# Kernel tuning notes

Hardware: AMD Instinct MI355X
Metric: run time of the kernel (lower is better)

The kernel has to match this reference:

```python
import jax, jax.numpy as jnp
import numpy as np

DIM = 1024
HEADS = 16
DIM_HEAD = 64
INNER = HEADS * DIM_HEAD  # 1024
FF_INNER = 4 * DIM        # 4096
EPS = 1e-5


def _ln(t, gamma):
    mu = jnp.mean(t, axis=-1, keepdims=True)
    var = jnp.var(t, axis=-1, keepdims=True)
    return (t - mu) * jax.lax.rsqrt(var + EPS) * gamma


def setup_inputs() -> dict:
    key = jax.random.key(0)
    ks = jax.random.split(key, 8)
    B, N = 4, 1024
    s = 0.02
    return {
        "x": jax.random.normal(ks[0], (B, N, DIM), dtype=jnp.float32),
        "y": jax.random.normal(ks[1], (B, N, DIM), dtype=jnp.float32),
        "g1": jnp.ones((DIM,), dtype=jnp.float32),
        "g2": jnp.ones((DIM,), dtype=jnp.float32),
        "g_out": jnp.ones((DIM,), dtype=jnp.float32),
        "Wq": jax.random.normal(ks[2], (DIM, INNER), dtype=jnp.float32) * s,
        "Wkv": jax.random.normal(ks[3], (DIM, 2 * DIM_HEAD), dtype=jnp.float32) * s,
        "Wo": jax.random.normal(ks[4], (INNER, DIM), dtype=jnp.float32) * s,
        "Wff1": jax.random.normal(ks[5], (DIM, 2 * FF_INNER), dtype=jnp.float32) * s,
        "Wff2": jax.random.normal(ks[6], (FF_INNER, DIM), dtype=jnp.float32) * s,
    }


def reference(x, y, g1, g2, g_out, Wq, Wkv, Wo, Wff1, Wff2):
    B, N, _ = x.shape
    scale = DIM_HEAD ** -0.5
    xn = _ln(x, g1)
    yn = _ln(y, g2)  # note: torch code rebinds y = norm2(y); residual & FF use normed y
    # multi-query attention: per-head queries, single shared k/v head
    q = (xn @ Wq).reshape(B, N, HEADS, DIM_HEAD).transpose(0, 2, 1, 3) * scale  # b h n d
    kv = yn @ Wkv  # b j (2d)
    k, v = kv[..., :DIM_HEAD], kv[..., DIM_HEAD:]
    sim = jnp.einsum('bhid,bjd->bhij', q, k)
    attn = jax.nn.softmax(sim, axis=-1)  # torch code subtracts amax then softmax; identical math
    out = jnp.einsum('bhij,bjd->bhid', attn, v)
    out = out.transpose(0, 2, 1, 3).reshape(B, N, INNER)
    out = out @ Wo
    out = _ln(out + yn, g_out)
    # SwiGLU FFN on normed y: first half is value, second half is gate
    h = yn @ Wff1
    val, gate = h[..., :FF_INNER], h[..., FF_INNER:]
    ff = (jax.nn.silu(gate) * val) @ Wff2
    return out + ff
```

## Files before the change

### kernel.cpp

```cpp
#include <hip/hip_runtime.h>
#include <hip/hip_bf16.h>


typedef __attribute__((ext_vector_type(8))) short bf16x8;
typedef __attribute__((ext_vector_type(4))) short s16x4;
typedef __attribute__((ext_vector_type(4))) float f32x4;

__device__ __forceinline__ short f2b(float f) {
  union { float f; unsigned u; } v; v.f = f;
  unsigned r = (v.u + 0x7fffu + ((v.u >> 16) & 1u)) >> 16;
  return (short)r;
}

__device__ __forceinline__ void gload16(const short* g, short* l) {
  __builtin_amdgcn_global_load_lds(
      (const __attribute__((address_space(1))) void*)g,
      (__attribute__((address_space(3))) void*)l, 16, 0, 0);
}

__global__ __launch_bounds__(256) void cvtT_kernel(const float* __restrict__ in,
                                                   short* __restrict__ out,
                                                   int K, int N) {
  __shared__ float tile[32][33];
  int n0 = blockIdx.x * 32, k0 = blockIdx.y * 32;
  int tx = threadIdx.x & 7, ty = threadIdx.x >> 3;
  float4 v = *(const float4*)&in[(size_t)(k0 + ty) * N + n0 + tx * 4];
  tile[ty][tx * 4 + 0] = v.x;
  tile[ty][tx * 4 + 1] = v.y;
  tile[ty][tx * 4 + 2] = v.z;
  tile[ty][tx * 4 + 3] = v.w;
  __syncthreads();
  s16x4 o = { f2b(tile[tx * 4 + 0][ty]), f2b(tile[tx * 4 + 1][ty]),
              f2b(tile[tx * 4 + 2][ty]), f2b(tile[tx * 4 + 3][ty]) };
  *(s16x4*)&out[(size_t)(n0 + ty) * K + k0 + tx * 4] = o;
}

__global__ __launch_bounds__(256) void ln_kernel(const float* __restrict__ in,
                                                 const float* __restrict__ gamma,
                                                 short* __restrict__ out16,
                                                 float* __restrict__ out32) {
  int row = blockIdx.x;
  int t = threadIdx.x;
  float4 v = ((const float4*)(in + (size_t)row * 1024))[t];
  float s  = v.x + v.y + v.z + v.w;
  float sq = v.x*v.x + v.y*v.y + v.z*v.z + v.w*v.w;
  __shared__ float ssum[256], ssq[256];
  ssum[t] = s; ssq[t] = sq;
  __syncthreads();
  for (int o = 128; o > 0; o >>= 1) {
    if (t < o) { ssum[t] += ssum[t + o]; ssq[t] += ssq[t + o]; }
    __syncthreads();
  }
  float mu  = ssum[0] * (1.0f / 1024.0f);
  float var = ssq[0] * (1.0f / 1024.0f) - mu * mu;
  float rs  = rsqrtf(var + 1e-5f);
  float4 g = ((const float4*)gamma)[t];
  float o0 = (v.x - mu) * rs * g.x;
  float o1 = (v.y - mu) * rs * g.y;
  float o2 = (v.z - mu) * rs * g.z;
  float o3 = (v.w - mu) * rs * g.w;
  if (out16) {
    s16x4 o = { f2b(o0), f2b(o1), f2b(o2), f2b(o3) };
    ((s16x4*)out16)[(size_t)row * 256 + t] = o;
  }
  if (out32) {
    float4 o = { o0, o1, o2, o3 };
    ((float4*)out32)[(size_t)row * 256 + t] = o;
  }
}

template<int EPI, int BM, int BN>
__global__ __launch_bounds__(256, 2) void gemm_ring(
    const short* __restrict__ A, const short* __restrict__ B,
    int M, int N, int Kstride, int Klen,
    short* __restrict__ out16, float* __restrict__ out32,
    const float* __restrict__ res, float scale)
{
  constexpr int DEPTH = 4;
  constexpr int FM = BM / 32;
  constexpr int FN = BN / 32;
  constexpr int AL = BM / 64;
  constexpr int BL = BN / 64;
  __shared__ __align__(16) short As[DEPTH][BM * 32];
  __shared__ __align__(16) short Bs[DEPTH][BN * 32];

  int t = threadIdx.x;
  int lane = t & 63, wave = t >> 6;
  int wm = wave >> 1, wn = wave & 1;
  int lrow = lane & 15, lgrp = lane >> 4;
  int m0 = blockIdx.y * BM, n0 = blockIdx.x * BN;
  int kbase = blockIdx.z * Klen;

  int srow = lane >> 2, scol = (lane & 3) * 8;
  const short* gA = A + (size_t)(m0 + wave * 16 + srow) * Kstride + kbase + scol;
  const short* gB = B + (size_t)(n0 + wave * 16 + srow) * Kstride + kbase + scol;

  auto STAGE = [&](int slot, int kt) {
    int k0 = kt * 32;
#pragma unroll
    for (int i = 0; i < AL; i++)
      gload16(gA + (size_t)(i * 64) * Kstride + k0, &As[slot][(i * 4 + wave) * 512]);
#pragma unroll
    for (int j = 0; j < BL; j++)
      gload16(gB + (size_t)(j * 64) * Kstride + k0, &Bs[slot][(j * 4 + wave) * 512]);
  };

  f32x4 acc[FM][FN];
  const f32x4 zero = { 0.f, 0.f, 0.f, 0.f };
#pragma unroll
  for (int i = 0; i < FM; i++)
#pragma unroll
    for (int j = 0; j < FN; j++) acc[i][j] = zero;

  int nt = Klen / 32;
#pragma unroll
  for (int p = 0; p < DEPTH - 1; p++) STAGE(p, p);

  int slot = 0, stage_slot = DEPTH - 1;
  for (int tI = 0; tI < nt; ++tI) {
    int rem = nt - 1 - tI;
    if constexpr (AL + BL == 4) {
      if (rem >= 2)      asm volatile("s_waitcnt vmcnt(8)" ::: "memory");
      else if (rem == 1) asm volatile("s_waitcnt vmcnt(4)" ::: "memory");
      else               asm volatile("s_waitcnt vmcnt(0)" ::: "memory");
    } else {
      if (rem >= 2)      asm volatile("s_waitcnt vmcnt(6)" ::: "memory");
      else if (rem == 1) asm volatile("s_waitcnt vmcnt(3)" ::: "memory");
      else               asm volatile("s_waitcnt vmcnt(0)" ::: "memory");
    }
    __builtin_amdgcn_s_barrier();
    __builtin_amdgcn_sched_barrier(0);

    if (tI + DEPTH - 1 < nt) STAGE(stage_slot, tI + DEPTH - 1);

    bf16x8 af[FM], bfr[FN];
#pragma unroll
    for (int mf = 0; mf < FM; mf++)
      af[mf] = *(const bf16x8*)&As[slot][(wm * (BM / 2) + mf * 16 + lrow) * 32 + lgrp * 8];
#pragma unroll
    for (int nf = 0; nf < FN; nf++)
      bfr[nf] = *(const bf16x8*)&Bs[slot][(wn * (BN / 2) + nf * 16 + lrow) * 32 + lgrp * 8];

    __builtin_amdgcn_s_setprio(1);
#pragma unroll
    for (int mf = 0; mf < FM; mf++)
#pragma unroll
      for (int nf = 0; nf < FN; nf++)
        acc[mf][nf] = __builtin_amdgcn_mfma_f32_16x16x32_bf16(af[mf], bfr[nf], acc[mf][nf], 0, 0, 0);
    __builtin_amdgcn_s_setprio(0);

    slot = (slot + 1 == DEPTH) ? 0 : slot + 1;
    stage_slot = (stage_slot + 1 == DEPTH) ? 0 : stage_slot + 1;
  }

#pragma unroll
  for (int mf = 0; mf < FM; mf++)
#pragma unroll
    for (int nf = 0; nf < FN; nf++)
#pragma unroll
      for (int r = 0; r < 4; r++) {
        int row = m0 + wm * (BM / 2) + mf * 16 + lgrp * 4 + r;
        int col = n0 + wn * (BN / 2) + nf * 16 + lrow;
        float v = acc[mf][nf][r];
        if (EPI == 0) {
          out16[(size_t)row * N + col] = f2b(v * scale);
        } else if (EPI == 1) {
          out32[(size_t)row * N + col] = v + res[(size_t)row * N + col];
        } else {
          out32[(size_t)blockIdx.z * M * N + (size_t)row * N + col] = v;
        }
      }
}

__global__ __launch_bounds__(256, 2) void gemm_ff1(
    const short* __restrict__ A, const short* __restrict__ B,
    short* __restrict__ out16)
{
  constexpr int K = 1024, NT = 16;
  __shared__ __align__(16) short As[2][128 * 64];
  __shared__ __align__(16) short Bv[2][64 * 64];
  __shared__ __align__(16) short Bg[2][64 * 64];

  int t = threadIdx.x;
  int lane = t & 63, wave = t >> 6;
  int wm = wave >> 1, wn = wave & 1;
  int lrow = lane & 15, lgrp = lane >> 4;
  int m0 = blockIdx.y * 128, n0 = blockIdx.x * 64;

  int r8 = lane >> 3;
  int schunk = ((lane & 7) ^ r8) * 8;
  const short* gA  = A + (size_t)(m0 + wave * 32 + r8) * K + schunk;
  const short* gBv = B + (size_t)(n0 + wave * 16 + r8) * K + schunk;
  const short* gBg = B + (size_t)(4096 + n0 + wave * 16 + r8) * K + schunk;

  auto STAGE = [&](int buf, int kt) {
    int k0 = kt * 64;
    gload16(gA + k0,                   &As[buf][(wave * 32 + 0) * 64]);
    gload16(gA + (size_t)8 * K + k0,   &As[buf][(wave * 32 + 8) * 64]);
    gload16(gA + (size_t)16 * K + k0,  &As[buf][(wave * 32 + 16) * 64]);
    gload16(gA + (size_t)24 * K + k0,  &As[buf][(wave * 32 + 24) * 64]);
    gload16(gBv + k0,                  &Bv[buf][(wave * 16 + 0) * 64]);
    gload16(gBv + (size_t)8 * K + k0,  &Bv[buf][(wave * 16 + 8) * 64]);
    gload16(gBg + k0,                  &Bg[buf][(wave * 16 + 0) * 64]);
    gload16(gBg + (size_t)8 * K + k0,  &Bg[buf][(wave * 16 + 8) * 64]);
  };

  f32x4 acc[4][2], acc2[4][2];
  const f32x4 zero = { 0.f, 0.f, 0.f, 0.f };
#pragma unroll
  for (int i = 0; i < 4; i++) {
    acc[i][0] = zero; acc[i][1] = zero; acc2[i][0] = zero; acc2[i][1] = zero;
  }

  int rc0 = ((lgrp) ^ (lrow & 7)) * 8;
  int rc1 = ((4 | lgrp) ^ (lrow & 7)) * 8;

  STAGE(0, 0);

  for (int tI = 0; tI < NT; ++tI) {
    int cur = tI & 1, nxt = cur ^ 1;

    asm volatile("s_waitcnt vmcnt(0)" ::: "memory");
    __builtin_amdgcn_s_barrier();
    __builtin_amdgcn_sched_barrier(0);

    if (tI + 1 < NT) STAGE(nxt, tI + 1);

    bf16x8 af0[4], af1[4], bvf[2], bgf[2];
#pragma unroll
    for (int mf = 0; mf < 4; mf++)
      af0[mf] = *(const bf16x8*)&As[cur][(wm * 64 + mf * 16 + lrow) * 64 + rc0];
    bvf[0] = *(const bf16x8*)&Bv[cur][(wn * 32 + lrow) * 64 + rc0];
    bvf[1] = *(const bf16x8*)&Bv[cur][(wn * 32 + 16 + lrow) * 64 + rc0];
    __builtin_amdgcn_s_setprio(1);
#pragma unroll
    for (int mf = 0; mf < 4; mf++) {
      acc[mf][0] = __builtin_amdgcn_mfma_f32_16x16x32_bf16(af0[mf], bvf[0], acc[mf][0], 0, 0, 0);
      acc[mf][1] = __builtin_amdgcn_mfma_f32_16x16x32_bf16(af0[mf], bvf[1], acc[mf][1], 0, 0, 0);
    }
#pragma unroll
    for (int mf = 0; mf < 4; mf++)
      af1[mf] = *(const bf16x8*)&As[cur][(wm * 64 + mf * 16 + lrow) * 64 + rc1];
    bvf[0] = *(const bf16x8*)&Bv[cur][(wn * 32 + lrow) * 64 + rc1];
    bvf[1] = *(const bf16x8*)&Bv[cur][(wn * 32 + 16 + lrow) * 64 + rc1];
#pragma unroll
    for (int mf = 0; mf < 4; mf++) {
      acc[mf][0] = __builtin_amdgcn_mfma_f32_16x16x32_bf16(af1[mf], bvf[0], acc[mf][0], 0, 0, 0);
      acc[mf][1] = __builtin_amdgcn_mfma_f32_16x16x32_bf16(af1[mf], bvf[1], acc[mf][1], 0, 0, 0);
    }
    bgf[0] = *(const bf16x8*)&Bg[cur][(wn * 32 + lrow) * 64 + rc0];
    bgf[1] = *(const bf16x8*)&Bg[cur][(wn * 32 + 16 + lrow) * 64 + rc0];
#pragma unroll
    for (int mf = 0; mf < 4; mf++) {
      acc2[mf][0] = __builtin_amdgcn_mfma_f32_16x16x32_bf16(af0[mf], bgf[0], acc2[mf][0], 0, 0, 0);
      acc2[mf][1] = __builtin_amdgcn_mfma_f32_16x16x32_bf16(af0[mf], bgf[1], acc2[mf][1], 0, 0, 0);
    }
    bgf[0] = *(const bf16x8*)&Bg[cur][(wn * 32 + lrow) * 64 + rc1];
    bgf[1] = *(const bf16x8*)&Bg[cur][(wn * 32 + 16 + lrow) * 64 + rc1];
#pragma unroll
    for (int mf = 0; mf < 4; mf++) {
      acc2[mf][0] = __builtin_amdgcn_mfma_f32_16x16x32_bf16(af1[mf], bgf[0], acc2[mf][0], 0, 0, 0);
      acc2[mf][1] = __builtin_amdgcn_mfma_f32_16x16x32_bf16(af1[mf], bgf[1], acc2[mf][1], 0, 0, 0);
    }
    __builtin_amdgcn_s_setprio(0);
  }

#pragma unroll
  for (int mf = 0; mf < 4; mf++)
#pragma unroll
    for (int nf = 0; nf < 2; nf++)
#pragma unroll
      for (int r = 0; r < 4; r++) {
        int row = m0 + wm * 64 + mf * 16 + lgrp * 4 + r;
        int col = n0 + wn * 32 + nf * 16 + lrow;
        float v = acc[mf][nf][r];
        float gate = acc2[mf][nf][r];
        float sig = 1.0f / (1.0f + __expf(-gate));
        out16[(size_t)row * 4096 + col] = f2b(v * gate * sig);
      }
}

__global__ __launch_bounds__(256) void kvred_kernel(const float* __restrict__ p,
                                                    short* __restrict__ out,
                                                    short* __restrict__ vT) {
  int i = blockIdx.x * 256 + threadIdx.x;
  const int S = 4096 * 128 / 4;
  float4 a = ((const float4*)p)[i];
  float4 b = ((const float4*)p)[i + S];
  float4 c = ((const float4*)p)[i + 2 * S];
  float4 d = ((const float4*)p)[i + 3 * S];
  s16x4 o = { f2b(a.x + b.x + c.x + d.x), f2b(a.y + b.y + c.y + d.y),
              f2b(a.z + b.z + c.z + d.z), f2b(a.w + b.w + c.w + d.w) };
  ((s16x4*)out)[i] = o;
  int row = i >> 5, col4 = i & 31;
  if (col4 >= 16) {
    int bb = row >> 10, n = row & 1023;
    int dbase = col4 * 4 - 64;
    short* vt = vT + ((size_t)(bb * 64 + dbase)) * 1024 + n;
    vt[0]        = o[0];
    vt[1024]     = o[1];
    vt[2048]     = o[2];
    vt[3072]     = o[3];
  }
}

__global__ __launch_bounds__(256) void attn_kernel(const short* __restrict__ q,
                                                   const short* __restrict__ kv,
                                                   const short* __restrict__ vT,
                                                   short* __restrict__ ao)
{
  __shared__ __align__(16) short Ks[2][64 * 64];
  __shared__ __align__(16) short Vt[2][64 * 64];
  __shared__ __align__(16) short Ps[4][32 * 64];

  int t = threadIdx.x;
  int lane = t & 63, wave = t >> 6;
  int lrow = lane & 15, lgrp = lane >> 4;
  int qt = blockIdx.x;
  int b = blockIdx.y >> 2, hg = blockIdx.y & 3;
  int h = hg * 4 + wave;

  char* Pb = (char*)Ps + wave * (32 * 64 * 2);

  int r8 = lane >> 3;
  int schunk = ((lane & 7) ^ r8) * 8;
  const short* gK = kv + ((size_t)(b * 1024 + wave * 16 + r8)) * 128 + schunk;
  const short* gV = vT + ((size_t)(b * 64 + wave * 16 + r8)) * 1024 + schunk;

  auto STAGE = [&](int buf, int j0) {
    gload16(gK + (size_t)(j0 + 0) * 128, &Ks[buf][(wave * 16 + 0) * 64]);
    gload16(gK + (size_t)(j0 + 8) * 128, &Ks[buf][(wave * 16 + 8) * 64]);
    gload16(gV + j0,                     &Vt[buf][(wave * 16 + 0) * 64]);
    gload16(gV + (size_t)8 * 1024 + j0,  &Vt[buf][(wave * 16 + 8) * 64]);
  };

  bf16x8 qf[2][2];
  const short* qb = q + ((size_t)(b * 1024 + qt * 32)) * 1024 + h * 64;
#pragma unroll
  for (int mf = 0; mf < 2; mf++)
#pragma unroll
    for (int kk = 0; kk < 2; kk++)
      qf[mf][kk] = *(const bf16x8*)&qb[(size_t)(mf * 16 + lrow) * 1024 + kk * 32 + lgrp * 8];

  f32x4 oacc[2][4];
  float m_[2][4], l_[2][4];
  const f32x4 zero = { 0.f, 0.f, 0.f, 0.f };
#pragma unroll
  for (int i = 0; i < 2; i++)
#pragma unroll
    for (int j = 0; j < 4; j++) { oacc[i][j] = zero; }
#pragma unroll
  for (int i = 0; i < 2; i++)
#pragma unroll
    for (int r = 0; r < 4; r++) { m_[i][r] = -3.0e38f; l_[i][r] = 0.f; }

  STAGE(0, 0);

  for (int tI = 0; tI < 16; ++tI) {
    int cur = tI & 1;
    int j0 = tI * 64;
    __builtin_amdgcn_s_barrier();
    __builtin_amdgcn_sched_barrier(0);
    if (tI + 1 < 16) STAGE(cur ^ 1, j0 + 64);
    __builtin_amdgcn_sched_barrier(0);
    if (tI + 1 < 16) asm volatile("s_waitcnt vmcnt(4)" ::: "memory");
    else             asm volatile("s_waitcnt vmcnt(0)" ::: "memory");
    __builtin_amdgcn_s_barrier();
    __builtin_amdgcn_sched_barrier(0);

    bf16x8 kf[4][2];
#pragma unroll
    for (int nf = 0; nf < 4; nf++) {
      int row = nf * 16 + lrow;
      kf[nf][0] = *(const bf16x8*)&Ks[cur][row * 64 + ((lgrp ^ (row & 7)) * 8)];
      kf[nf][1] = *(const bf16x8*)&Ks[cur][row * 64 + (((4 | lgrp) ^ (row & 7)) * 8)];
    }
    f32x4 sacc[2][4];
#pragma unroll
    for (int i = 0; i < 2; i++)
#pragma unroll
      for (int j = 0; j < 4; j++) sacc[i][j] = zero;
    __builtin_amdgcn_s_setprio(1);
#pragma unroll
    for (int mf = 0; mf < 2; mf++)
#pragma unroll
      for (int nf = 0; nf < 4; nf++)
#pragma unroll
        for (int kk = 0; kk < 2; kk++)
          sacc[mf][nf] = __builtin_amdgcn_mfma_f32_16x16x32_bf16(qf[mf][kk], kf[nf][kk], sacc[mf][nf], 0, 0, 0);
    __builtin_amdgcn_s_setprio(0);

    float pmax[2][4];
    bool okd = true;
#pragma unroll
    for (int mf = 0; mf < 2; mf++)
#pragma unroll
      for (int r = 0; r < 4; r++) {
        float pm = fmaxf(fmaxf(sacc[mf][0][r], sacc[mf][1][r]),
                         fmaxf(sacc[mf][2][r], sacc[mf][3][r]));
        pmax[mf][r] = pm;
        okd = okd && (pm <= m_[mf][r] + 8.0f);
      }
    if (__all(okd)) {
#pragma unroll
      for (int mf = 0; mf < 2; mf++)
#pragma unroll
        for (int r = 0; r < 4; r++) {
          int row = mf * 16 + lgrp * 4 + r, sw = (row & 7) << 4;
          float al = 0.f;
#pragma unroll
          for (int nf = 0; nf < 4; nf++) {
            float p = __expf(sacc[mf][nf][r] - m_[mf][r]);
            *(short*)(Pb + row * 128 + (((nf * 16 + lrow) * 2) ^ sw)) = f2b(p);
            al += p;
          }
          l_[mf][r] += al;
        }
    } else {
#pragma unroll
      for (int mf = 0; mf < 2; mf++)
#pragma unroll
        for (int r = 0; r < 4; r++) {
          float mx = pmax[mf][r];
#pragma unroll
          for (int o = 8; o >= 1; o >>= 1) mx = fmaxf(mx, __shfl_xor(mx, o));
          float mnew = fmaxf(m_[mf][r], mx);
          float corr = __expf(m_[mf][r] - mnew);
          int row = mf * 16 + lgrp * 4 + r, sw = (row & 7) << 4;
          float al = 0.f;
#pragma unroll
          for (int nf = 0; nf < 4; nf++) {
            float p = __expf(sacc[mf][nf][r] - mnew);
            *(short*)(Pb + row * 128 + (((nf * 16 + lrow) * 2) ^ sw)) = f2b(p);
            al += p;
          }
          l_[mf][r] = l_[mf][r] * corr + al;
          m_[mf][r] = mnew;
#pragma unroll
          for (int nf = 0; nf < 4; nf++) oacc[mf][nf][r] *= corr;
        }
    }

    bf16x8 vf[4][2], pfr[2][2];
#pragma unroll
    for (int nf = 0; nf < 4; nf++) {
      int row = nf * 16 + lrow;
      vf[nf][0] = *(const bf16x8*)&Vt[cur][row * 64 + ((lgrp ^ (row & 7)) * 8)];
      vf[nf][1] = *(const bf16x8*)&Vt[cur][row * 64 + (((4 | lgrp) ^ (row & 7)) * 8)];
    }
#pragma unroll
    for (int mf = 0; mf < 2; mf++) {
      int row = mf * 16 + lrow, sw = (row & 7) << 4;
      pfr[mf][0] = *(const bf16x8*)(Pb + row * 128 + ((lgrp * 16) ^ sw));
      pfr[mf][1] = *(const bf16x8*)(Pb + row * 128 + ((64 + lgrp * 16) ^ sw));
    }
    __builtin_amdgcn_s_setprio(1);
#pragma unroll
    for (int mf = 0; mf < 2; mf++)
#pragma unroll
      for (int nf = 0; nf < 4; nf++)
#pragma unroll
        for (int kk = 0; kk < 2; kk++)
          oacc[mf][nf] = __builtin_amdgcn_mfma_f32_16x16x32_bf16(pfr[mf][kk], vf[nf][kk], oacc[mf][nf], 0, 0, 0);
    __builtin_amdgcn_s_setprio(0);
  }

#pragma unroll
  for (int mf = 0; mf < 2; mf++)
#pragma unroll
    for (int r = 0; r < 4; r++) {
      float ls = l_[mf][r];
#pragma unroll
      for (int o = 8; o >= 1; o >>= 1) ls += __shfl_xor(ls, o);
      float inv = 1.0f / ls;
      int qrow = qt * 32 + mf * 16 + lgrp * 4 + r;
#pragma unroll
      for (int nf = 0; nf < 4; nf++) {
        float val = oacc[mf][nf][r] * inv;
        ao[((size_t)(b * 1024 + qrow)) * 1024 + h * 64 + nf * 16 + lrow] = f2b(val);
      }
    }
}

extern "C" void kernel_launch(void* const* d_in, const int* in_sizes, int n_in,
                              void* d_out, int out_size, void* d_ws, size_t ws_size,
                              hipStream_t stream) {
  const float* x     = (const float*)d_in[0];
  const float* y     = (const float*)d_in[1];
  const float* g1    = (const float*)d_in[2];
  const float* g2    = (const float*)d_in[3];
  const float* g_out = (const float*)d_in[4];
  const float* Wq    = (const float*)d_in[5];
  const float* Wkv   = (const float*)d_in[6];
  const float* Wo    = (const float*)d_in[7];
  const float* Wff1  = (const float*)d_in[8];
  const float* Wff2  = (const float*)d_in[9];

  char* ws = (char*)d_ws;
  size_t off = 0;
  auto alloc = [&](size_t bytes) { char* p = ws + off; off += bytes; return p; };
  short* wqT    = (short*)alloc((size_t)1024 * 1024 * 2);
  short* wkvT   = (short*)alloc((size_t)128 * 1024 * 2);
  short* woT    = (short*)alloc((size_t)1024 * 1024 * 2);
  short* wff1T  = (short*)alloc((size_t)8192 * 1024 * 2);
  short* wff2T  = (short*)alloc((size_t)1024 * 4096 * 2);
  short* xn16   = (short*)alloc((size_t)4096 * 1024 * 2);
  short* yn16   = (short*)alloc((size_t)4096 * 1024 * 2);
  float* ynf    = (float*)alloc((size_t)4096 * 1024 * 4);
  short* q16    = (short*)alloc((size_t)4096 * 1024 * 2);
  short* kv16   = (short*)alloc((size_t)4096 * 128 * 2);
  short* vT16   = (short*)alloc((size_t)4 * 64 * 1024 * 2);
  short* ao16   = (short*)alloc((size_t)4096 * 1024 * 2);
  float* lnout  = (float*)alloc((size_t)4096 * 1024 * 4);
  short* act16  = (short*)alloc((size_t)4096 * 4096 * 2);
  float* kvpart = (float*)alloc((size_t)4 * 4096 * 128 * 4);
  float* outf   = (float*)d_out;

  cvtT_kernel<<<dim3(1024 / 32, 1024 / 32), 256, 0, stream>>>(Wq,   wqT,   1024, 1024);
  cvtT_kernel<<<dim3(128 / 32, 1024 / 32),  256, 0, stream>>>(Wkv,  wkvT,  1024, 128);
  cvtT_kernel<<<dim3(1024 / 32, 1024 / 32), 256, 0, stream>>>(Wo,   woT,   1024, 1024);
  cvtT_kernel<<<dim3(8192 / 32, 1024 / 32), 256, 0, stream>>>(Wff1, wff1T, 1024, 8192);
  cvtT_kernel<<<dim3(1024 / 32, 4096 / 32), 256, 0, stream>>>(Wff2, wff2T, 4096, 1024);

  ln_kernel<<<4096, 256, 0, stream>>>(x, g1, xn16, nullptr);
  ln_kernel<<<4096, 256, 0, stream>>>(y, g2, yn16, ynf);

  gemm_ring<0, 64, 128><<<dim3(8, 64), 256, 0, stream>>>(
      xn16, wqT, 4096, 1024, 1024, 1024, q16, nullptr, nullptr, 0.125f);
  gemm_ring<3, 64, 128><<<dim3(1, 64, 4), 256, 0, stream>>>(
      yn16, wkvT, 4096, 128, 1024, 256, nullptr, kvpart, nullptr, 1.0f);
  kvred_kernel<<<512, 256, 0, stream>>>(kvpart, kv16, vT16);

  attn_kernel<<<dim3(32, 16), 256, 0, stream>>>(q16, kv16, vT16, ao16);

  gemm_ring<1, 64, 128><<<dim3(8, 64), 256, 0, stream>>>(
      ao16, woT, 4096, 1024, 1024, 1024, nullptr, outf, ynf, 1.0f);

  ln_kernel<<<4096, 256, 0, stream>>>(outf, g_out, nullptr, lnout);

  gemm_ff1<<<dim3(64, 32), 256, 0, stream>>>(yn16, wff1T, act16);

  gemm_ring<1, 64, 128><<<dim3(8, 64), 256, 0, stream>>>(
      act16, wff2T, 4096, 1024, 4096, 4096, nullptr, outf, lnout, 1.0f);
}
```

Baseline: 292.9 us.

## Split attention over two KV halves and merge with a combine kernel

Attention blocks now each process half of the key/value sequence (grid z=2), writing unnormalized fp32 partial outputs plus per-row max and sum. A new combine kernel rescales and merges the two partials into the bf16 attention output. This doubles the number of blocks to improve GPU occupancy, at the cost of extra fp32 partial traffic and an added kernel launch.

```diff
diff --git a/kernel.cpp b/kernel.cpp
--- a/kernel.cpp
+++ b/kernel.cpp
@@ -307,7 +307,8 @@
 __global__ __launch_bounds__(256) void attn_kernel(const short* __restrict__ q,
                                                    const short* __restrict__ kv,
                                                    const short* __restrict__ vT,
-                                                   short* __restrict__ ao)
+                                                   float* __restrict__ of,
+                                                   float* __restrict__ ml)
 {
   __shared__ __align__(16) short Ks[2][64 * 64];
   __shared__ __align__(16) short Vt[2][64 * 64];
@@ -318,14 +319,16 @@
   int lrow = lane & 15, lgrp = lane >> 4;
   int qt = blockIdx.x;
   int b = blockIdx.y >> 2, hg = blockIdx.y & 3;
+  int z = blockIdx.z;
   int h = hg * 4 + wave;
+  int kvbase = z * 512;
 
   char* Pb = (char*)Ps + wave * (32 * 64 * 2);
 
   int r8 = lane >> 3;
   int schunk = ((lane & 7) ^ r8) * 8;
-  const short* gK = kv + ((size_t)(b * 1024 + wave * 16 + r8)) * 128 + schunk;
-  const short* gV = vT + ((size_t)(b * 64 + wave * 16 + r8)) * 1024 + schunk;
+  const short* gK = kv + ((size_t)(b * 1024 + kvbase + wave * 16 + r8)) * 128 + schunk;
+  const short* gV = vT + ((size_t)(b * 64 + wave * 16 + r8)) * 1024 + kvbase + schunk;
 
   auto STAGE = [&](int buf, int j0) {
     gload16(gK + (size_t)(j0 + 0) * 128, &Ks[buf][(wave * 16 + 0) * 64]);
@@ -356,15 +359,15 @@
 
   STAGE(0, 0);
 
-  for (int tI = 0; tI < 16; ++tI) {
+  for (int tI = 0; tI < 8; ++tI) {
     int cur = tI & 1;
     int j0 = tI * 64;
     __builtin_amdgcn_s_barrier();
     __builtin_amdgcn_sched_barrier(0);
-    if (tI + 1 < 16) STAGE(cur ^ 1, j0 + 64);
+    if (tI + 1 < 8) STAGE(cur ^ 1, j0 + 64);
     __builtin_amdgcn_sched_barrier(0);
-    if (tI + 1 < 16) asm volatile("s_waitcnt vmcnt(4)" ::: "memory");
-    else             asm volatile("s_waitcnt vmcnt(0)" ::: "memory");
+    if (tI + 1 < 8) asm volatile("s_waitcnt vmcnt(4)" ::: "memory");
+    else            asm volatile("s_waitcnt vmcnt(0)" ::: "memory");
     __builtin_amdgcn_s_barrier();
     __builtin_amdgcn_sched_barrier(0);
 
@@ -465,6 +468,7 @@
     __builtin_amdgcn_s_setprio(0);
   }
 
+  float* ob = of + (size_t)z * 4096 * 1024;
 #pragma unroll
   for (int mf = 0; mf < 2; mf++)
 #pragma unroll
@@ -472,14 +476,36 @@
       float ls = l_[mf][r];
 #pragma unroll
       for (int o = 8; o >= 1; o >>= 1) ls += __shfl_xor(ls, o);
-      float inv = 1.0f / ls;
       int qrow = qt * 32 + mf * 16 + lgrp * 4 + r;
 #pragma unroll
-      for (int nf = 0; nf < 4; nf++) {
-        float val = oacc[mf][nf][r] * inv;
-        ao[((size_t)(b * 1024 + qrow)) * 1024 + h * 64 + nf * 16 + lrow] = f2b(val);
+      for (int nf = 0; nf < 4; nf++)
+        ob[((size_t)(b * 1024 + qrow)) * 1024 + h * 64 + nf * 16 + lrow] = oacc[mf][nf][r];
+      if (lrow == 0) {
+        float2* mlp = (float2*)ml + ((size_t)z * 4096 + b * 1024 + qrow) * 16 + h;
+        *mlp = make_float2(m_[mf][r], ls);
       }
     }
+}
+
+__global__ __launch_bounds__(256) void attn_combine(const float* __restrict__ of,
+                                                    const float* __restrict__ ml,
+                                                    short* __restrict__ ao) {
+  int i = blockIdx.x * 256 + threadIdx.x;
+  int row = i >> 8;
+  int c4 = i & 255;
+  int h = c4 >> 4;
+  const float2* mlp = (const float2*)ml;
+  float2 ml0 = mlp[((size_t)0 * 4096 + row) * 16 + h];
+  float2 ml1 = mlp[((size_t)1 * 4096 + row) * 16 + h];
+  float m = fmaxf(ml0.x, ml1.x);
+  float w0 = __expf(ml0.x - m), w1 = __expf(ml1.x - m);
+  float inv = 1.0f / (ml0.y * w0 + ml1.y * w1);
+  const int S = 4096 * 1024 / 4;
+  float4 a = ((const float4*)of)[i];
+  float4 b = ((const float4*)of)[i + S];
+  s16x4 o = { f2b((a.x * w0 + b.x * w1) * inv), f2b((a.y * w0 + b.y * w1) * inv),
+              f2b((a.z * w0 + b.z * w1) * inv), f2b((a.w * w0 + b.w * w1) * inv) };
+  ((s16x4*)ao)[i] = o;
 }
 
 extern "C" void kernel_launch(void* const* d_in, const int* in_sizes, int n_in,
@@ -514,6 +540,11 @@
   float* lnout  = (float*)alloc((size_t)4096 * 1024 * 4);
   short* act16  = (short*)alloc((size_t)4096 * 4096 * 2);
   float* kvpart = (float*)alloc((size_t)4 * 4096 * 128 * 4);
+  float* ofbuf  = (float*)kvpart;
+  float* ofb    = (float*)alloc((size_t)2 * 4096 * 1024 * 4 - (size_t)4 * 4096 * 128 * 4);
+  (void)ofbuf; (void)ofb;
+  float* of     = kvpart;
+  float* mlb    = (float*)alloc((size_t)2 * 4096 * 16 * 2 * 4);
   float* outf   = (float*)d_out;
 
   cvtT_kernel<<<dim3(1024 / 32, 1024 / 32), 256, 0, stream>>>(Wq,   wqT,   1024, 1024);
@@ -531,7 +562,8 @@
       yn16, wkvT, 4096, 128, 1024, 256, nullptr, kvpart, nullptr, 1.0f);
   kvred_kernel<<<512, 256, 0, stream>>>(kvpart, kv16, vT16);
 
-  attn_kernel<<<dim3(32, 16), 256, 0, stream>>>(q16, kv16, vT16, ao16);
+  attn_kernel<<<dim3(32, 16, 2), 256, 0, stream>>>(q16, kv16, vT16, of, mlb);
+  attn_combine<<<4096, 256, 0, stream>>>(of, mlb, ao16);
 
   gemm_ring<1, 64, 128><<<dim3(8, 64), 256, 0, stream>>>(
       ao16, woT, 4096, 1024, 1024, 1024, nullptr, outf, ynf, 1.0f);
```

After: 307.1 us. +4.8%, slower.
